# Kernel optimization log

Measured on AMD Instinct MI355X. Metric: run time of the kernel, lower is better.

Reference implementation:

```python
import jax, jax.numpy as jnp
import numpy as np

N = 50000      # nodes
E = 800000     # edges (before self-loops)
IN_DIM = 128
HID = 64
OUT = 32
HEADS = 8
BN_EPS = 1e-5
NEG_SLOPE = 0.2  # PyG GATConv default


def setup_inputs() -> dict:
    key = jax.random.key(0)
    ks = jax.random.split(key, 24)
    g = lambda k, shape, fan_in: (jax.random.normal(k, shape, jnp.float32) / np.sqrt(fan_in))
    return {
        "x": jax.random.normal(ks[0], (N, IN_DIM), jnp.float32),
        "edge_index": jax.random.randint(ks[1], (2, E), 0, N, dtype=jnp.int64),
        # GCN1
        "gcn1_w": g(ks[2], (IN_DIM, HID), IN_DIM),
        "gcn1_b": jnp.zeros((HID,), jnp.float32),
        # BN1 (eval mode running stats)
        "bn1_gamma": jnp.ones((HID,), jnp.float32),
        "bn1_beta": jnp.zeros((HID,), jnp.float32),
        "bn1_mean": 0.1 * jax.random.normal(ks[3], (HID,), jnp.float32),
        "bn1_var": 0.5 + jax.random.uniform(ks[4], (HID,), jnp.float32),
        # GAT1: heads=8, per-head out=HID, concat=False -> mean over heads
        "gat1_w": g(ks[5], (HID, HEADS * HID), HID),
        "gat1_asrc": g(ks[6], (HEADS, HID), HID),
        "gat1_adst": g(ks[7], (HEADS, HID), HID),
        "gat1_b": jnp.zeros((HID,), jnp.float32),
        # GCN2
        "gcn2_w": g(ks[8], (HID, HID), HID),
        "gcn2_b": jnp.zeros((HID,), jnp.float32),
        # BN2
        "bn2_gamma": jnp.ones((HID,), jnp.float32),
        "bn2_beta": jnp.zeros((HID,), jnp.float32),
        "bn2_mean": 0.1 * jax.random.normal(ks[9], (HID,), jnp.float32),
        "bn2_var": 0.5 + jax.random.uniform(ks[10], (HID,), jnp.float32),
        # GAT2: heads=8, per-head out=OUT, concat=False
        "gat2_w": g(ks[11], (HID, HEADS * OUT), HID),
        "gat2_asrc": g(ks[12], (HEADS, OUT), OUT),
        "gat2_adst": g(ks[13], (HEADS, OUT), OUT),
        "gat2_b": jnp.zeros((OUT,), jnp.float32),
    }


def _gcn(x, src, dst, w, b, n):
    # PyG GCNConv: x @ W, symmetric norm with self-loops (src/dst already include them)
    h = x @ w
    deg = jax.ops.segment_sum(jnp.ones(src.shape[0], x.dtype), dst, num_segments=n)
    dinv = jnp.where(deg > 0, jax.lax.rsqrt(jnp.maximum(deg, 1.0)), 0.0)
    coef = dinv[src] * dinv[dst]                     # [E']
    out = jax.ops.segment_sum(coef[:, None] * h[src], dst, num_segments=n)
    return out + b


def _gat(x, src, dst, w, a_src, a_dst, b, n, heads, ch):
    # PyG GATConv (concat=False): mean over heads, softmax over incoming edges per dst
    h = (x @ w).reshape(n, heads, ch)                # [N,H,C]
    es = jnp.einsum('nhc,hc->nh', h, a_src)          # alpha_src per node
    ed = jnp.einsum('nhc,hc->nh', h, a_dst)
    e = jax.nn.leaky_relu(es[src] + ed[dst], NEG_SLOPE)  # [E',H]
    m = jax.ops.segment_max(e, dst, num_segments=n)
    m = jnp.where(jnp.isfinite(m), m, 0.0)
    ex = jnp.exp(e - m[dst])
    denom = jax.ops.segment_sum(ex, dst, num_segments=n)
    alpha = ex / (denom[dst] + 1e-16)                # [E',H]
    out = jnp.zeros((n, ch), x.dtype)
    for hd in range(heads):  # fixed small head loop keeps peak edge memory at [E',C]
        msg = alpha[:, hd, None] * h[src, hd]        # [E',C]
        out = out + jax.ops.segment_sum(msg, dst, num_segments=n)
    return out / heads + b


def _bn_eval(x, gamma, beta, mean, var):
    return (x - mean) * jax.lax.rsqrt(var + BN_EPS) * gamma + beta


def reference(x, edge_index,
              gcn1_w, gcn1_b, bn1_gamma, bn1_beta, bn1_mean, bn1_var,
              gat1_w, gat1_asrc, gat1_adst, gat1_b,
              gcn2_w, gcn2_b, bn2_gamma, bn2_beta, bn2_mean, bn2_var,
              gat2_w, gat2_asrc, gat2_adst, gat2_b):
    n = x.shape[0]
    loops = jnp.arange(n, dtype=edge_index.dtype)
    src = jnp.concatenate([edge_index[0], loops])    # self-loops (PyG default)
    dst = jnp.concatenate([edge_index[1], loops])

    h = _gcn(x, src, dst, gcn1_w, gcn1_b, n)
    h = jax.nn.relu(_bn_eval(h, bn1_gamma, bn1_beta, bn1_mean, bn1_var))
    h = jax.nn.relu(_gat(h, src, dst, gat1_w, gat1_asrc, gat1_adst, gat1_b, n, HEADS, HID))
    h = _gcn(h, src, dst, gcn2_w, gcn2_b, n)
    h = jax.nn.relu(_bn_eval(h, bn2_gamma, bn2_beta, bn2_mean, bn2_var))
    h = _gat(h, src, dst, gat2_w, gat2_asrc, gat2_adst, gat2_b, n, HEADS, OUT)
    return jax.nn.log_softmax(h, axis=1)
```

## Files before the change

### kernel.cpp

```cpp
#include <hip/hip_runtime.h>
#include <hip/hip_bf16.h>

#define NN 50000
#define NE 800000
#define IND 128
#define NH 8
#define EBLK 256
#define EPB 3125
#define NBUK 391
#define NBUKP 392
#define GH (NBUKP * EBLK)

typedef __hip_bfloat16 bf16;
typedef __attribute__((ext_vector_type(8))) short short8;
typedef __attribute__((ext_vector_type(8))) __bf16 bf16x8;
typedef __attribute__((ext_vector_type(4))) float floatx4;
typedef __attribute__((ext_vector_type(2))) float floatx2;

static __device__ __forceinline__ short f2bf_bits(float f) {
    unsigned u = __float_as_uint(f);
    u = (u + 0x7fffu + ((u >> 16) & 1u)) >> 16;
    return (short)u;
}
static __device__ __forceinline__ float bf2f(bf16 v) { return __bfloat162float(v); }
static __device__ __forceinline__ floatx2 up2(unsigned av) {
    floatx2 r;
    r.x = __uint_as_float(av << 16);
    r.y = __uint_as_float(av & 0xffff0000u);
    return r;
}
static __device__ __forceinline__ unsigned pk2(float a, float b) {
    return (unsigned)(unsigned short)f2bf_bits(a) | ((unsigned)(unsigned short)f2bf_bits(b) << 16);
}

__global__ __launch_bounds__(256) void bin_count_kernel(const int* __restrict__ edst,
        int* __restrict__ ghist) {
    __shared__ int h[NBUKP];
    const int tid = threadIdx.x, blk = blockIdx.x;
    for (int b = tid; b < NBUKP; b += 256) h[b] = 0;
    __syncthreads();
    const int e0 = blk * EPB;
    for (int e = e0 + tid; e < e0 + EPB; e += 256)
        atomicAdd(&h[edst[e] >> 7], 1);
    __syncthreads();
    for (int b = tid; b < NBUKP; b += 256)
        ghist[b * EBLK + blk] = h[b];
}
__global__ __launch_bounds__(256) void scang1_kernel(const int* __restrict__ src,
        int* __restrict__ pre, int* __restrict__ bsum, int n) {
    __shared__ int sh[256];
    const int tid = threadIdx.x;
    const int idx = blockIdx.x * 256 + tid;
    int c = (idx < n) ? src[idx] : 0;
    sh[tid] = c; __syncthreads();
    int val = c;
#pragma unroll
    for (int off = 1; off < 256; off <<= 1) {
        int t = (tid >= off) ? sh[tid - off] : 0;
        __syncthreads();
        val += t; sh[tid] = val;
        __syncthreads();
    }
    if (idx < n) pre[idx] = val - c;
    if (tid == 255) bsum[blockIdx.x] = val;
}
__global__ __launch_bounds__(512) void scang2_kernel(int* __restrict__ bsum, int nb) {
    __shared__ int sh[512];
    const int tid = threadIdx.x;
    int v = (tid < nb) ? bsum[tid] : 0;
    sh[tid] = v; __syncthreads();
    int val = v;
#pragma unroll
    for (int off = 1; off < 512; off <<= 1) {
        int t = (tid >= off) ? sh[tid - off] : 0;
        __syncthreads();
        val += t; sh[tid] = val;
        __syncthreads();
    }
    if (tid < nb) bsum[tid] = val - v;
}
__global__ __launch_bounds__(256) void bin_scatter_kernel(const int* __restrict__ esrc,
        const int* __restrict__ edst, const int* __restrict__ gpre,
        const int* __restrict__ gbsum, unsigned* __restrict__ ebuf) {
    __shared__ int cur[NBUKP];
    const int tid = threadIdx.x, blk = blockIdx.x;
    for (int b = tid; b < NBUKP; b += 256) {
        int i = b * EBLK + blk;
        cur[b] = gpre[i] + gbsum[i >> 8];
    }
    __syncthreads();
    const int e0 = blk * EPB;
    for (int e = e0 + tid; e < e0 + EPB; e += 256) {
        int d = edst[e], s = esrc[e];
        int pos = atomicAdd(&cur[d >> 7], 1);
        ebuf[pos] = ((unsigned)(d & 127) << 16) | (unsigned)s;
    }
}
__global__ __launch_bounds__(256) void bucket_finalize_kernel(const unsigned* __restrict__ ebuf,
        const int* __restrict__ gpre, const int* __restrict__ gbsum,
        int* __restrict__ rowptr, float* __restrict__ dinv, int* __restrict__ csrc) {
    __shared__ int lh[128], lcur[128], sc[256];
    const int bu = blockIdx.x, tid = threadIdx.x;
    const int seg_beg = gpre[bu * EBLK] + gbsum[bu];
    const int seg_end = gpre[(bu + 1) * EBLK] + gbsum[bu + 1];
    if (tid < 128) lh[tid] = 0;
    __syncthreads();
    for (int i = seg_beg + tid; i < seg_end; i += 256)
        atomicAdd(&lh[ebuf[i] >> 16], 1);
    __syncthreads();
    int c = (tid < 128) ? lh[tid] : 0;
    sc[tid] = c; __syncthreads();
    int val = c;
#pragma unroll
    for (int off = 1; off < 256; off <<= 1) {
        int t = (tid >= off) ? sc[tid - off] : 0;
        __syncthreads();
        val += t; sc[tid] = val;
        __syncthreads();
    }
    int excl = val - c;
    if (tid < 128) {
        lcur[tid] = excl;
        int node = bu * 128 + tid;
        if (node < NN) {
            rowptr[node] = seg_beg + excl;
            dinv[node] = rsqrtf((float)c + 1.f);
        }
    }
    if (bu == 0 && tid == 0) rowptr[NN] = NE;
    __syncthreads();
    for (int i = seg_beg + tid; i < seg_end; i += 256) {
        unsigned u = ebuf[i];
        int pos = atomicAdd(&lcur[u >> 16], 1);
        csrc[seg_beg + pos] = (int)(u & 0xffffu);
    }
}

__global__ __launch_bounds__(256) void prep_all_kernel(
        const float* __restrict__ gcn1_w, const float* __restrict__ gcn2_w,
        const float* __restrict__ gat1_w, const float* __restrict__ gat2_w,
        const float* __restrict__ as1, const float* __restrict__ ad1,
        const float* __restrict__ as2, const float* __restrict__ ad2,
        bf16* __restrict__ wT1, bf16* __restrict__ wT2,
        bf16* __restrict__ wgT1, bf16* __restrict__ wgT2,
        float* __restrict__ was1, float* __restrict__ wad1,
        float* __restrict__ was2, float* __restrict__ wad2) {
    int idx = blockIdx.x * 256 + threadIdx.x;
    if (idx < 8192) {
        int m = idx >> 7, k = idx & 127;
        ((short*)wT1)[idx] = f2bf_bits(gcn1_w[(long)k * 64 + m]);
    } else if (idx < 12288) {
        int i = idx - 8192;
        int m = i >> 6, k = i & 63;
        ((short*)wT2)[i] = f2bf_bits(gcn2_w[(long)k * 64 + m]);
    } else if (idx < 45056) {
        int i = idx - 12288;
        int m = i >> 9, k = i & 511;
        int h = k >> 6, c = k & 63;
        ((short*)wgT1)[i] = f2bf_bits(gat1_w[(long)c * 512 + h * 64 + m]);
    } else if (idx < 77824) {
        int i = idx - 45056;
        int m = i >> 9, k = i & 511;
        int h = k >> 6, c = k & 63;
        ((short*)wgT2)[i] = (m < 32) ? f2bf_bits(gat2_w[(long)c * 256 + h * 32 + m]) : (short)0;
    } else if (idx < 78336) {
        int i = idx - 77824;
        int h = i >> 6, c = i & 63;
        const float* wrow = gat1_w + (long)c * 512 + h * 64;
        float s = 0.f, d = 0.f;
        for (int cc = 0; cc < 64; ++cc) {
            float w = wrow[cc];
            s += w * as1[h * 64 + cc];
            d += w * ad1[h * 64 + cc];
        }
        was1[i] = s; wad1[i] = d;
    } else if (idx < 78848) {
        int i = idx - 78336;
        int h = i >> 6, c = i & 63;
        const float* wrow = gat2_w + (long)c * 256 + h * 32;
        float s = 0.f, d = 0.f;
        for (int cc = 0; cc < 32; ++cc) {
            float w = wrow[cc];
            s += w * as2[h * 32 + cc];
            d += w * ad2[h * 32 + cc];
        }
        was2[i] = s; wad2[i] = d;
    }
}

template<int K, int EPI, bool AF32>
__global__ __launch_bounds__(256) void mm2_kernel(const void* __restrict__ A,
        const bf16* __restrict__ wT, void* __restrict__ C,
        const float* __restrict__ bias, const float* __restrict__ rowscale,
        int nrows, int M) {
    const int row0 = blockIdx.x * 64;
    const int tid = threadIdx.x;
    const int lane = tid & 63, wave = tid >> 6;
    const int lr = lane & 15, q = lane >> 4;
    const int row = row0 + wave * 16 + lr;
    const bool rok = row < nrows;
    constexpr int NC = (EPI == 4) ? 2 : 4;
    floatx4 acc[NC] = {};
#pragma unroll 4
    for (int k0 = 0; k0 < K; k0 += 32) {
        short8 av = {0, 0, 0, 0, 0, 0, 0, 0};
        if (rok) {
            if (AF32) {
                const float* apf = (const float*)A + (long)row * K + q * 8 + k0;
                floatx4 va = *(const floatx4*)apf;
                floatx4 vb = *(const floatx4*)(apf + 4);
#pragma unroll
                for (int j = 0; j < 4; ++j) { av[j] = f2bf_bits(va[j]); av[4 + j] = f2bf_bits(vb[j]); }
            } else {
                av = *(const short8*)((const short*)A + (long)row * K + q * 8 + k0);
            }
        }
        bf16x8 a = __builtin_bit_cast(bf16x8, av);
#pragma unroll
        for (int c = 0; c < NC; ++c) {
            bf16x8 b = __builtin_bit_cast(bf16x8,
                *(const short8*)((const short*)wT + (long)(c * 16 + lr) * K + k0 + q * 8));
            acc[c] = __builtin_amdgcn_mfma_f32_16x16x32_bf16(a, b, acc[c], 0, 0, 0);
        }
    }
    if (EPI == 4) {
#pragma unroll
        for (int r = 0; r < 4; ++r) {
            int orow = row0 + wave * 16 + q * 4 + r;
            float v0 = acc[0][r] * 0.125f + bias[lr];
            float v1 = acc[1][r] * 0.125f + bias[16 + lr];
            float m = fmaxf(v0, v1);
#pragma unroll
            for (int off = 1; off < 16; off <<= 1) m = fmaxf(m, __shfl_xor(m, off));
            float s = __expf(v0 - m) + __expf(v1 - m);
#pragma unroll
            for (int off = 1; off < 16; off <<= 1) s += __shfl_xor(s, off);
            float ls = m + logf(s);
            if (orow < nrows) {
                ((float*)C)[(long)orow * 32 + lr] = v0 - ls;
                ((float*)C)[(long)orow * 32 + 16 + lr] = v1 - ls;
            }
        }
        return;
    }
#pragma unroll
    for (int c = 0; c < NC; ++c)
#pragma unroll
        for (int r = 0; r < 4; ++r) {
            int orow = row0 + wave * 16 + q * 4 + r;
            int col = c * 16 + lr;
            if (orow < nrows && col < M) {
                long o = (long)orow * M + col;
                float v = acc[c][r];
                if (EPI == 0) ((float*)C)[o] = v;
                else if (EPI == 2) {
                    v = v * 0.125f + bias[col];
                    ((bf16*)C)[o] = __float2bfloat16(fmaxf(v, 0.f));
                } else {
                    ((bf16*)C)[o] = __float2bfloat16(rowscale[orow] * v);
                }
            }
        }
}

__global__ __launch_bounds__(256) void gcn_fused_kernel(const int* __restrict__ rowptr,
        const int* __restrict__ csrc, const float* __restrict__ dinv,
        const bf16* __restrict__ hin, const float* __restrict__ b,
        const float* __restrict__ gamma, const float* __restrict__ beta,
        const float* __restrict__ mean, const float* __restrict__ var,
        bf16* __restrict__ actout) {
    const int node = blockIdx.x * 4 + (threadIdx.x >> 6);
    if (node >= NN) return;
    const int lane = threadIdx.x & 63;
    const int eslot = lane >> 5, cp = lane & 31;
    const int beg = rowptr[node], end = rowptr[node + 1];
    const float di = dinv[node];
    floatx2 acc2 = {0.f, 0.f};
#pragma unroll 2
    for (int ei = beg + eslot; ei < end; ei += 2) {
        int s = csrc[ei];
        unsigned av = *(const unsigned*)((const unsigned short*)hin + (long)s * 64 + 2 * cp);
        acc2 += up2(av);
    }
    acc2.x += __shfl_xor(acc2.x, 32);
    acc2.y += __shfl_xor(acc2.y, 32);
    {
        unsigned sv = *(const unsigned*)((const unsigned short*)hin + (long)node * 64 + 2 * cp);
        acc2 += up2(sv);
    }
    int c0 = 2 * cp, c1 = c0 + 1;
    float x0 = acc2.x * di + b[c0];
    float x1 = acc2.y * di + b[c1];
    x0 = (x0 - mean[c0]) * rsqrtf(var[c0] + 1e-5f) * gamma[c0] + beta[c0];
    x1 = (x1 - mean[c1]) * rsqrtf(var[c1] + 1e-5f) * gamma[c1] + beta[c1];
    if (eslot == 0)
        *(unsigned*)((unsigned short*)actout + (long)node * 64 + c0) =
            pk2(fmaxf(x0, 0.f), fmaxf(x1, 0.f));
}

__global__ __launch_bounds__(256) void scores_kernel(const bf16* __restrict__ actb,
        const float* __restrict__ was, const float* __restrict__ wad,
        float* __restrict__ es, float* __restrict__ ed, int n) {
    const int node = blockIdx.x * 4 + (threadIdx.x >> 6);
    if (node >= n) return;
    const int lane = threadIdx.x & 63;
    const int h = lane >> 3, cg = lane & 7;
    short8 a8 = *(const short8*)((const short*)actb + (long)node * 64 + cg * 8);
    const float* wsp = was + h * 64 + cg * 8;
    const float* wdp = wad + h * 64 + cg * 8;
    floatx4 ws0 = *(const floatx4*)wsp, ws1 = *(const floatx4*)(wsp + 4);
    floatx4 wd0 = *(const floatx4*)wdp, wd1 = *(const floatx4*)(wdp + 4);
    float s = 0.f, d = 0.f;
#pragma unroll
    for (int j = 0; j < 4; ++j) {
        float v0 = bf2f(__builtin_bit_cast(bf16, a8[j]));
        float v1 = bf2f(__builtin_bit_cast(bf16, a8[4 + j]));
        s += v0 * ws0[j] + v1 * ws1[j];
        d += v0 * wd0[j] + v1 * wd1[j];
    }
#pragma unroll
    for (int off = 1; off < 8; off <<= 1) {
        s += __shfl_xor(s, off);
        d += __shfl_xor(d, off);
    }
    if (cg == 0) { es[node * NH + h] = s; ed[node * NH + h] = d; }
}

__global__ __launch_bounds__(256) void gat_agg_kernel(const int* __restrict__ rowptr,
        const int* __restrict__ csrc, const float* __restrict__ es, const float* __restrict__ ed,
        const bf16* __restrict__ actb, bf16* __restrict__ agg) {
    __shared__ __align__(16) float salpha[4][512];
    __shared__ int ssrcs[4][64];
    __shared__ __align__(16) float sself[4][8];
    const int wv = threadIdx.x >> 6;
    const int node = blockIdx.x * 4 + wv;
    if (node >= NN) return;
    const int lane = threadIdx.x & 63;
    const int h = lane & 7, slot = lane >> 3;
    const int beg = rowptr[node], end = rowptr[node + 1];
    const int deg = end - beg;
    const float edr = ed[node * NH + h];

    float selfe = es[node * NH + h] + edr;
    selfe = selfe > 0.f ? selfe : 0.2f * selfe;

    if (deg <= 64) {
        float ex_r[8]; int s_r[8];
        float den = 0.f;
#pragma unroll
        for (int b = 0; b < 8; ++b) {
            ex_r[b] = 0.f; s_r[b] = 0;
            int k = b * 8 + slot;
            if (k < deg) {
                int s = csrc[beg + k];
                s_r[b] = s;
                float e = es[s * NH + h] + edr;
                e = e > 0.f ? e : 0.2f * e;
                ex_r[b] = __expf(e - selfe);
                den += ex_r[b];
            }
        }
        den += __shfl_xor(den, 8);
        den += __shfl_xor(den, 16);
        den += __shfl_xor(den, 32);
        const float invden = 1.f / (den + 1.f);

#pragma unroll
        for (int b = 0; b < 8; ++b)
            salpha[wv][b * 64 + lane] = ex_r[b] * invden;
        if (h == 0) {
#pragma unroll
            for (int b = 0; b < 8; ++b)
                ssrcs[wv][b * 8 + slot] = s_r[b];
        }
        if (slot == 0) sself[wv][h] = invden;

        const int hq = lane >> 5, cp = lane & 31;
        floatx2 acc2[4] = {};
#pragma unroll 4
        for (int k = 0; k < deg; ++k) {
            int s = ssrcs[wv][k];
            unsigned av = *(const unsigned*)((const unsigned short*)actb + (long)s * 64 + 2 * cp);
            floatx2 a2 = up2(av);
            floatx4 al = *(const floatx4*)&salpha[wv][(k >> 3) * 64 + (k & 7) * 8 + hq * 4];
            acc2[0] += a2 * al[0]; acc2[1] += a2 * al[1];
            acc2[2] += a2 * al[2]; acc2[3] += a2 * al[3];
        }
        {
            unsigned sv = *(const unsigned*)((const unsigned short*)actb + (long)node * 64 + 2 * cp);
            floatx2 a2 = up2(sv);
            floatx4 sa = *(const floatx4*)&sself[wv][hq * 4];
            acc2[0] += a2 * sa[0]; acc2[1] += a2 * sa[1];
            acc2[2] += a2 * sa[2]; acc2[3] += a2 * sa[3];
        }
#pragma unroll
        for (int j = 0; j < 4; ++j)
            *(unsigned*)((unsigned short*)agg + (long)node * 512 + (hq * 4 + j) * 64 + 2 * cp) =
                pk2(acc2[j].x, acc2[j].y);
    } else {
        float acc[NH] = {0.f, 0.f, 0.f, 0.f, 0.f, 0.f, 0.f, 0.f};
        float den = 0.f;
        for (int base = beg; base < end; base += 8) {
            int ei = base + slot;
            if (ei < end) {
                int s = csrc[ei];
                float e = es[s * NH + h] + edr;
                e = e > 0.f ? e : 0.2f * e;
                den += __expf(e - selfe);
            }
        }
        den += __shfl_xor(den, 8);
        den += __shfl_xor(den, 16);
        den += __shfl_xor(den, 32);
        const float invden = 1.f / (den + 1.f);
        for (int base = beg; base < end; base += 8) {
            int ei = base + slot;
            float al = 0.f; int sl = 0;
            if (ei < end) {
                sl = csrc[ei];
                float e = es[sl * NH + h] + edr;
                e = e > 0.f ? e : 0.2f * e;
                al = __expf(e - selfe) * invden;
            }
            salpha[wv][lane] = al;
            if (h == 0) ssrcs[wv][slot] = sl;
            int ecnt = end - base; if (ecnt > 8) ecnt = 8;
            for (int j = 0; j < ecnt; ++j) {
                int s = ssrcs[wv][j];
                float a = bf2f(actb[(long)s * 64 + lane]);
                floatx4 al0 = *(const floatx4*)&salpha[wv][j * 8];
                floatx4 al1 = *(const floatx4*)&salpha[wv][j * 8 + 4];
                acc[0] += al0[0] * a; acc[1] += al0[1] * a;
                acc[2] += al0[2] * a; acc[3] += al0[3] * a;
                acc[4] += al1[0] * a; acc[5] += al1[1] * a;
                acc[6] += al1[2] * a; acc[7] += al1[3] * a;
            }
        }
        {
            if (slot == 0) sself[wv][h] = invden;
            float a = bf2f(actb[(long)node * 64 + lane]);
            floatx4 s0 = *(const floatx4*)&sself[wv][0];
            floatx4 s1 = *(const floatx4*)&sself[wv][4];
            acc[0] += s0[0] * a; acc[1] += s0[1] * a;
            acc[2] += s0[2] * a; acc[3] += s0[3] * a;
            acc[4] += s1[0] * a; acc[5] += s1[1] * a;
            acc[6] += s1[2] * a; acc[7] += s1[3] * a;
        }
#pragma unroll
        for (int hh = 0; hh < NH; ++hh)
            agg[(long)node * 512 + hh * 64 + lane] = __float2bfloat16(acc[hh]);
    }
}

extern "C" void kernel_launch(void* const* d_in, const int* in_sizes, int n_in,
                              void* d_out, int out_size, void* d_ws, size_t ws_size,
                              hipStream_t stream) {
    const float* x        = (const float*)d_in[0];
    const int*   eidx     = (const int*)d_in[1];
    const float* gcn1_w   = (const float*)d_in[2];
    const float* gcn1_b   = (const float*)d_in[3];
    const float* bn1_g    = (const float*)d_in[4];
    const float* bn1_b    = (const float*)d_in[5];
    const float* bn1_m    = (const float*)d_in[6];
    const float* bn1_v    = (const float*)d_in[7];
    const float* gat1_w   = (const float*)d_in[8];
    const float* gat1_as  = (const float*)d_in[9];
    const float* gat1_ad  = (const float*)d_in[10];
    const float* gat1_b   = (const float*)d_in[11];
    const float* gcn2_w   = (const float*)d_in[12];
    const float* gcn2_b   = (const float*)d_in[13];
    const float* bn2_g    = (const float*)d_in[14];
    const float* bn2_b    = (const float*)d_in[15];
    const float* bn2_m    = (const float*)d_in[16];
    const float* bn2_v    = (const float*)d_in[17];
    const float* gat2_w   = (const float*)d_in[18];
    const float* gat2_as  = (const float*)d_in[19];
    const float* gat2_ad  = (const float*)d_in[20];
    const float* gat2_b   = (const float*)d_in[21];
    float* out = (float*)d_out;

    const int* esrc = eidx;
    const int* edst = eidx + NE;

    float* ws = (float*)d_ws;
    int*      ghist  = (int*)ws;
    int*      gpre   = ghist + GH;
    int*      gbsum  = gpre + GH;
    unsigned* ebuf   = (unsigned*)(gbsum + 512);
    int*      rowptr = (int*)(ebuf + NE);
    int*      csrc   = rowptr + 50048;
    float*    dinv   = (float*)(csrc + NE);
    float*    es     = dinv + 50048;
    float*    ed     = es + 400000;
    float*    was1   = ed + 400000;
    float*    wad1   = was1 + 512;
    float*    was2   = wad1 + 512;
    float*    wad2   = was2 + 512;
    bf16*     wT1    = (bf16*)(wad2 + 512);
    bf16*     wT2    = wT1 + 64 * 128;
    bf16*     wgT1   = wT2 + 64 * 64;
    bf16*     wgT2   = wgT1 + 64 * 512;
    bf16*     actb   = wgT2 + 64 * 512;
    bf16*     mmbf   = actb + (size_t)NN * 64;
    bf16*     agg    = mmbf + (size_t)NN * 64;

    auto cdiv = [](long a, long b) { return (int)((a + b - 1) / b); };
    const int GB = cdiv(NN, 64);
    const int NB = cdiv(NN, 4);

    bin_count_kernel<<<EBLK, 256, 0, stream>>>(edst, ghist);
    scang1_kernel<<<GH / 256, 256, 0, stream>>>(ghist, gpre, gbsum, GH);
    scang2_kernel<<<1, 512, 0, stream>>>(gbsum, GH / 256);
    bin_scatter_kernel<<<EBLK, 256, 0, stream>>>(esrc, edst, gpre, gbsum, ebuf);
    bucket_finalize_kernel<<<NBUK, 256, 0, stream>>>(ebuf, gpre, gbsum, rowptr, dinv, csrc);

    prep_all_kernel<<<cdiv(78848, 256), 256, 0, stream>>>(
        gcn1_w, gcn2_w, gat1_w, gat2_w, gat1_as, gat1_ad, gat2_as, gat2_ad,
        wT1, wT2, wgT1, wgT2, was1, wad1, was2, wad2);

    mm2_kernel<IND, 3, true><<<GB, 256, 0, stream>>>(x, wT1, mmbf, nullptr, dinv, NN, 64);
    gcn_fused_kernel<<<NB, 256, 0, stream>>>(rowptr, csrc, dinv, mmbf,
        gcn1_b, bn1_g, bn1_b, bn1_m, bn1_v, actb);

    scores_kernel<<<NB, 256, 0, stream>>>(actb, was1, wad1, es, ed, NN);
    gat_agg_kernel<<<NB, 256, 0, stream>>>(rowptr, csrc, es, ed, actb, agg);
    mm2_kernel<512, 2, false><<<GB, 256, 0, stream>>>(agg, wgT1, actb, gat1_b, nullptr, NN, 64);

    mm2_kernel<64, 3, false><<<GB, 256, 0, stream>>>(actb, wT2, mmbf, nullptr, dinv, NN, 64);
    gcn_fused_kernel<<<NB, 256, 0, stream>>>(rowptr, csrc, dinv, mmbf,
        gcn2_b, bn2_g, bn2_b, bn2_m, bn2_v, actb);

    scores_kernel<<<NB, 256, 0, stream>>>(actb, was2, wad2, es, ed, NN);
    gat_agg_kernel<<<NB, 256, 0, stream>>>(rowptr, csrc, es, ed, actb, agg);
    mm2_kernel<512, 4, false><<<GB, 256, 0, stream>>>(agg, wgT2, out, gat2_b, nullptr, NN, 32);
}
```

Measured before the change: 405.5 us.

## Merge prep into bin-count, fold bucket scan into consumers, batch gather loads

Fuses the weight-prep kernel into the bin-count launch as extra blocks and removes the single-block second-level scan by having each scatter and finalize block recompute the 392-bucket prefix in shared memory. This cuts two kernel launches and their serialization. The GCN and GAT aggregation loops are restructured to issue four independent neighbour gathers before accumulating, with masked or clamped indices, to raise memory-level parallelism. In exchange every scatter/finalize block does redundant scan work, and padded edges add a few wasted loads.

```diff
diff --git a/kernel.cpp b/kernel.cpp
--- a/kernel.cpp
+++ b/kernel.cpp
@@ -10,6 +10,7 @@
 #define NBUK 391
 #define NBUKP 392
 #define GH (NBUKP * EBLK)
+#define PREPB 308
 
 typedef __hip_bfloat16 bf16;
 typedef __attribute__((ext_vector_type(8))) short short8;
@@ -33,19 +34,93 @@
     return (unsigned)(unsigned short)f2bf_bits(a) | ((unsigned)(unsigned short)f2bf_bits(b) << 16);
 }
 
-__global__ __launch_bounds__(256) void bin_count_kernel(const int* __restrict__ edst,
-        int* __restrict__ ghist) {
-    __shared__ int h[NBUKP];
-    const int tid = threadIdx.x, blk = blockIdx.x;
-    for (int b = tid; b < NBUKP; b += 256) h[b] = 0;
+static __device__ __forceinline__ void scan_buckets(const int* __restrict__ bsum,
+        int* sp, int* gb, int tid) {
+    int v0 = (2 * tid < NBUKP) ? bsum[2 * tid] : 0;
+    int v1 = (2 * tid + 1 < NBUKP) ? bsum[2 * tid + 1] : 0;
+    int c = v0 + v1;
+    sp[tid] = c; __syncthreads();
+    int val = c;
+#pragma unroll
+    for (int off = 1; off < 256; off <<= 1) {
+        int t = (tid >= off) ? sp[tid - off] : 0;
+        __syncthreads();
+        val += t; sp[tid] = val;
+        __syncthreads();
+    }
+    int pex = val - c;
+    gb[2 * tid] = pex;
+    gb[2 * tid + 1] = pex + v0;
     __syncthreads();
-    const int e0 = blk * EPB;
-    for (int e = e0 + tid; e < e0 + EPB; e += 256)
-        atomicAdd(&h[edst[e] >> 7], 1);
-    __syncthreads();
-    for (int b = tid; b < NBUKP; b += 256)
-        ghist[b * EBLK + blk] = h[b];
-}
+}
+
+__global__ __launch_bounds__(256) void bin_count_prep_kernel(const int* __restrict__ edst,
+        int* __restrict__ ghist,
+        const float* __restrict__ gcn1_w, const float* __restrict__ gcn2_w,
+        const float* __restrict__ gat1_w, const float* __restrict__ gat2_w,
+        const float* __restrict__ as1, const float* __restrict__ ad1,
+        const float* __restrict__ as2, const float* __restrict__ ad2,
+        bf16* __restrict__ wT1, bf16* __restrict__ wT2,
+        bf16* __restrict__ wgT1, bf16* __restrict__ wgT2,
+        float* __restrict__ was1, float* __restrict__ wad1,
+        float* __restrict__ was2, float* __restrict__ wad2) {
+    __shared__ int hsh[NBUKP];
+    const int tid = threadIdx.x;
+    if (blockIdx.x < EBLK) {
+        const int blk = blockIdx.x;
+        for (int b = tid; b < NBUKP; b += 256) hsh[b] = 0;
+        __syncthreads();
+        const int e0 = blk * EPB;
+        for (int e = e0 + tid; e < e0 + EPB; e += 256)
+            atomicAdd(&hsh[edst[e] >> 7], 1);
+        __syncthreads();
+        for (int b = tid; b < NBUKP; b += 256)
+            ghist[b * EBLK + blk] = hsh[b];
+    } else {
+        int idx = (blockIdx.x - EBLK) * 256 + tid;
+        if (idx < 8192) {
+            int m = idx >> 7, k = idx & 127;
+            ((short*)wT1)[idx] = f2bf_bits(gcn1_w[(long)k * 64 + m]);
+        } else if (idx < 12288) {
+            int i = idx - 8192;
+            int m = i >> 6, k = i & 63;
+            ((short*)wT2)[i] = f2bf_bits(gcn2_w[(long)k * 64 + m]);
+        } else if (idx < 45056) {
+            int i = idx - 12288;
+            int m = i >> 9, k = i & 511;
+            int h = k >> 6, c = k & 63;
+            ((short*)wgT1)[i] = f2bf_bits(gat1_w[(long)c * 512 + h * 64 + m]);
+        } else if (idx < 77824) {
+            int i = idx - 45056;
+            int m = i >> 9, k = i & 511;
+            int h = k >> 6, c = k & 63;
+            ((short*)wgT2)[i] = (m < 32) ? f2bf_bits(gat2_w[(long)c * 256 + h * 32 + m]) : (short)0;
+        } else if (idx < 78336) {
+            int i = idx - 77824;
+            int h = i >> 6, c = i & 63;
+            const float* wrow = gat1_w + (long)c * 512 + h * 64;
+            float s = 0.f, d = 0.f;
+            for (int cc = 0; cc < 64; ++cc) {
+                float w = wrow[cc];
+                s += w * as1[h * 64 + cc];
+                d += w * ad1[h * 64 + cc];
+            }
+            was1[i] = s; wad1[i] = d;
+        } else if (idx < 78848) {
+            int i = idx - 78336;
+            int h = i >> 6, c = i & 63;
+            const float* wrow = gat2_w + (long)c * 256 + h * 32;
+            float s = 0.f, d = 0.f;
+            for (int cc = 0; cc < 32; ++cc) {
+                float w = wrow[cc];
+                s += w * as2[h * 32 + cc];
+                d += w * ad2[h * 32 + cc];
+            }
+            was2[i] = s; wad2[i] = d;
+        }
+    }
+}
+
 __global__ __launch_bounds__(256) void scang1_kernel(const int* __restrict__ src,
         int* __restrict__ pre, int* __restrict__ bsum, int n) {
     __shared__ int sh[256];
@@ -64,30 +139,16 @@
     if (idx < n) pre[idx] = val - c;
     if (tid == 255) bsum[blockIdx.x] = val;
 }
-__global__ __launch_bounds__(512) void scang2_kernel(int* __restrict__ bsum, int nb) {
-    __shared__ int sh[512];
-    const int tid = threadIdx.x;
-    int v = (tid < nb) ? bsum[tid] : 0;
-    sh[tid] = v; __syncthreads();
-    int val = v;
-#pragma unroll
-    for (int off = 1; off < 512; off <<= 1) {
-        int t = (tid >= off) ? sh[tid - off] : 0;
-        __syncthreads();
-        val += t; sh[tid] = val;
-        __syncthreads();
-    }
-    if (tid < nb) bsum[tid] = val - v;
-}
+
 __global__ __launch_bounds__(256) void bin_scatter_kernel(const int* __restrict__ esrc,
         const int* __restrict__ edst, const int* __restrict__ gpre,
-        const int* __restrict__ gbsum, unsigned* __restrict__ ebuf) {
+        const int* __restrict__ bsum, unsigned* __restrict__ ebuf) {
     __shared__ int cur[NBUKP];
+    __shared__ int sp[256], gb[512];
     const int tid = threadIdx.x, blk = blockIdx.x;
-    for (int b = tid; b < NBUKP; b += 256) {
-        int i = b * EBLK + blk;
-        cur[b] = gpre[i] + gbsum[i >> 8];
-    }
+    scan_buckets(bsum, sp, gb, tid);
+    for (int b = tid; b < NBUKP; b += 256)
+        cur[b] = gpre[b * EBLK + blk] + gb[b];
     __syncthreads();
     const int e0 = blk * EPB;
     for (int e = e0 + tid; e < e0 + EPB; e += 256) {
@@ -96,13 +157,16 @@
         ebuf[pos] = ((unsigned)(d & 127) << 16) | (unsigned)s;
     }
 }
+
 __global__ __launch_bounds__(256) void bucket_finalize_kernel(const unsigned* __restrict__ ebuf,
-        const int* __restrict__ gpre, const int* __restrict__ gbsum,
+        const int* __restrict__ gpre, const int* __restrict__ bsum,
         int* __restrict__ rowptr, float* __restrict__ dinv, int* __restrict__ csrc) {
     __shared__ int lh[128], lcur[128], sc[256];
+    __shared__ int sp[256], gb[512];
     const int bu = blockIdx.x, tid = threadIdx.x;
-    const int seg_beg = gpre[bu * EBLK] + gbsum[bu];
-    const int seg_end = gpre[(bu + 1) * EBLK] + gbsum[bu + 1];
+    scan_buckets(bsum, sp, gb, tid);
+    const int seg_beg = gpre[bu * EBLK] + gb[bu];
+    const int seg_end = gpre[(bu + 1) * EBLK] + gb[bu + 1];
     if (tid < 128) lh[tid] = 0;
     __syncthreads();
     for (int i = seg_beg + tid; i < seg_end; i += 256)
@@ -133,58 +197,6 @@
         unsigned u = ebuf[i];
         int pos = atomicAdd(&lcur[u >> 16], 1);
         csrc[seg_beg + pos] = (int)(u & 0xffffu);
-    }
-}
-
-__global__ __launch_bounds__(256) void prep_all_kernel(
-        const float* __restrict__ gcn1_w, const float* __restrict__ gcn2_w,
-        const float* __restrict__ gat1_w, const float* __restrict__ gat2_w,
-        const float* __restrict__ as1, const float* __restrict__ ad1,
-        const float* __restrict__ as2, const float* __restrict__ ad2,
-        bf16* __restrict__ wT1, bf16* __restrict__ wT2,
-        bf16* __restrict__ wgT1, bf16* __restrict__ wgT2,
-        float* __restrict__ was1, float* __restrict__ wad1,
-        float* __restrict__ was2, float* __restrict__ wad2) {
-    int idx = blockIdx.x * 256 + threadIdx.x;
-    if (idx < 8192) {
-        int m = idx >> 7, k = idx & 127;
-        ((short*)wT1)[idx] = f2bf_bits(gcn1_w[(long)k * 64 + m]);
-    } else if (idx < 12288) {
-        int i = idx - 8192;
-        int m = i >> 6, k = i & 63;
-        ((short*)wT2)[i] = f2bf_bits(gcn2_w[(long)k * 64 + m]);
-    } else if (idx < 45056) {
-        int i = idx - 12288;
-        int m = i >> 9, k = i & 511;
-        int h = k >> 6, c = k & 63;
-        ((short*)wgT1)[i] = f2bf_bits(gat1_w[(long)c * 512 + h * 64 + m]);
-    } else if (idx < 77824) {
-        int i = idx - 45056;
-        int m = i >> 9, k = i & 511;
-        int h = k >> 6, c = k & 63;
-        ((short*)wgT2)[i] = (m < 32) ? f2bf_bits(gat2_w[(long)c * 256 + h * 32 + m]) : (short)0;
-    } else if (idx < 78336) {
-        int i = idx - 77824;
-        int h = i >> 6, c = i & 63;
-        const float* wrow = gat1_w + (long)c * 512 + h * 64;
-        float s = 0.f, d = 0.f;
-        for (int cc = 0; cc < 64; ++cc) {
-            float w = wrow[cc];
-            s += w * as1[h * 64 + cc];
-            d += w * ad1[h * 64 + cc];
-        }
-        was1[i] = s; wad1[i] = d;
-    } else if (idx < 78848) {
-        int i = idx - 78336;
-        int h = i >> 6, c = i & 63;
-        const float* wrow = gat2_w + (long)c * 256 + h * 32;
-        float s = 0.f, d = 0.f;
-        for (int cc = 0; cc < 32; ++cc) {
-            float w = wrow[cc];
-            s += w * as2[h * 32 + cc];
-            d += w * ad2[h * 32 + cc];
-        }
-        was2[i] = s; wad2[i] = d;
     }
 }
 
@@ -274,18 +286,34 @@
     const int lane = threadIdx.x & 63;
     const int eslot = lane >> 5, cp = lane & 31;
     const int beg = rowptr[node], end = rowptr[node + 1];
+    const int deg = end - beg;
     const float di = dinv[node];
+    const char* hp = (const char*)hin + 4 * cp;
     floatx2 acc2 = {0.f, 0.f};
-#pragma unroll 2
-    for (int ei = beg + eslot; ei < end; ei += 2) {
-        int s = csrc[ei];
-        unsigned av = *(const unsigned*)((const unsigned short*)hin + (long)s * 64 + 2 * cp);
-        acc2 += up2(av);
+    const int kup = (deg + 7) & ~7;
+    for (int k0 = 0; k0 < kup; k0 += 8) {
+        int s_[4]; float w_[4];
+#pragma unroll
+        for (int u = 0; u < 4; ++u) {
+            int ei = beg + k0 + 2 * u + eslot;
+            int ok = ei < end;
+            s_[u] = csrc[ok ? ei : beg];
+            w_[u] = ok ? 1.f : 0.f;
+        }
+        unsigned av_[4];
+#pragma unroll
+        for (int u = 0; u < 4; ++u)
+            av_[u] = *(const unsigned*)(hp + (long)s_[u] * 128);
+#pragma unroll
+        for (int u = 0; u < 4; ++u) {
+            floatx2 a2 = up2(av_[u]);
+            acc2 += a2 * w_[u];
+        }
     }
     acc2.x += __shfl_xor(acc2.x, 32);
     acc2.y += __shfl_xor(acc2.y, 32);
     {
-        unsigned sv = *(const unsigned*)((const unsigned short*)hin + (long)node * 64 + 2 * cp);
+        unsigned sv = *(const unsigned*)(hp + (long)node * 128);
         acc2 += up2(sv);
     }
     int c0 = 2 * cp, c1 = c0 + 1;
@@ -347,16 +375,19 @@
     if (deg <= 64) {
         float ex_r[8]; int s_r[8];
         float den = 0.f;
-#pragma unroll
-        for (int b = 0; b < 8; ++b) {
-            ex_r[b] = 0.f; s_r[b] = 0;
-            int k = b * 8 + slot;
-            if (k < deg) {
-                int s = csrc[beg + k];
-                s_r[b] = s;
-                float e = es[s * NH + h] + edr;
+        if (deg > 0) {
+            const int dm1 = deg - 1;
+#pragma unroll
+            for (int b = 0; b < 8; ++b) {
+                int k = b * 8 + slot;
+                s_r[b] = csrc[beg + (k < deg ? k : dm1)];
+            }
+#pragma unroll
+            for (int b = 0; b < 8; ++b) {
+                float e = es[s_r[b] * NH + h] + edr;
                 e = e > 0.f ? e : 0.2f * e;
-                ex_r[b] = __expf(e - selfe);
+                float ex = __expf(e - selfe);
+                ex_r[b] = (b * 8 + slot < deg) ? ex : 0.f;
                 den += ex_r[b];
             }
         }
@@ -367,27 +398,40 @@
 
 #pragma unroll
         for (int b = 0; b < 8; ++b)
-            salpha[wv][b * 64 + lane] = ex_r[b] * invden;
+            if (b * 8 < deg) salpha[wv][b * 64 + lane] = ex_r[b] * invden;
         if (h == 0) {
 #pragma unroll
             for (int b = 0; b < 8; ++b)
-                ssrcs[wv][b * 8 + slot] = s_r[b];
+                if (b * 8 < deg) ssrcs[wv][b * 8 + slot] = s_r[b];
         }
         if (slot == 0) sself[wv][h] = invden;
 
         const int hq = lane >> 5, cp = lane & 31;
+        const char* actp = (const char*)actb + 4 * cp;
+        const float* alp = &salpha[wv][hq * 4];
         floatx2 acc2[4] = {};
-#pragma unroll 4
-        for (int k = 0; k < deg; ++k) {
-            int s = ssrcs[wv][k];
-            unsigned av = *(const unsigned*)((const unsigned short*)actb + (long)s * 64 + 2 * cp);
-            floatx2 a2 = up2(av);
-            floatx4 al = *(const floatx4*)&salpha[wv][(k >> 3) * 64 + (k & 7) * 8 + hq * 4];
-            acc2[0] += a2 * al[0]; acc2[1] += a2 * al[1];
-            acc2[2] += a2 * al[2]; acc2[3] += a2 * al[3];
+        const int kup = (deg + 3) & ~3;
+        for (int k0 = 0; k0 < kup; k0 += 4) {
+            int s_[4];
+#pragma unroll
+            for (int u = 0; u < 4; ++u) s_[u] = ssrcs[wv][k0 + u];
+            unsigned av_[4];
+#pragma unroll
+            for (int u = 0; u < 4; ++u)
+                av_[u] = *(const unsigned*)(actp + (long)s_[u] * 128);
+            floatx4 al_[4];
+#pragma unroll
+            for (int u = 0; u < 4; ++u)
+                al_[u] = *(const floatx4*)(alp + (k0 + u) * 8);
+#pragma unroll
+            for (int u = 0; u < 4; ++u) {
+                floatx2 a2 = up2(av_[u]);
+                acc2[0] += a2 * al_[u][0]; acc2[1] += a2 * al_[u][1];
+                acc2[2] += a2 * al_[u][2]; acc2[3] += a2 * al_[u][3];
+            }
         }
         {
-            unsigned sv = *(const unsigned*)((const unsigned short*)actb + (long)node * 64 + 2 * cp);
+            unsigned sv = *(const unsigned*)(actp + (long)node * 128);
             floatx2 a2 = up2(sv);
             floatx4 sa = *(const floatx4*)&sself[wv][hq * 4];
             acc2[0] += a2 * sa[0]; acc2[1] += a2 * sa[1];
@@ -508,15 +552,12 @@
     const int GB = cdiv(NN, 64);
     const int NB = cdiv(NN, 4);
 
-    bin_count_kernel<<<EBLK, 256, 0, stream>>>(edst, ghist);
+    bin_count_prep_kernel<<<EBLK + PREPB, 256, 0, stream>>>(edst, ghist,
+        gcn1_w, gcn2_w, gat1_w, gat2_w, gat1_as, gat1_ad, gat2_as, gat2_ad,
+        wT1, wT2, wgT1, wgT2, was1, wad1, was2, wad2);
     scang1_kernel<<<GH / 256, 256, 0, stream>>>(ghist, gpre, gbsum, GH);
-    scang2_kernel<<<1, 512, 0, stream>>>(gbsum, GH / 256);
     bin_scatter_kernel<<<EBLK, 256, 0, stream>>>(esrc, edst, gpre, gbsum, ebuf);
     bucket_finalize_kernel<<<NBUK, 256, 0, stream>>>(ebuf, gpre, gbsum, rowptr, dinv, csrc);
-
-    prep_all_kernel<<<cdiv(78848, 256), 256, 0, stream>>>(
-        gcn1_w, gcn2_w, gat1_w, gat2_w, gat1_as, gat1_ad, gat2_as, gat2_ad,
-        wT1, wT2, wgT1, wgT2, was1, wad1, was2, wad2);
 
     mm2_kernel<IND, 3, true><<<GB, 256, 0, stream>>>(x, wT1, mmbf, nullptr, dinv, NN, 64);
     gcn_fused_kernel<<<NB, 256, 0, stream>>>(rowptr, csrc, dinv, mmbf,
```

Result: faster. 378.9 us (-6.6%).
